# Kernel optimization log

Measured on AMD Instinct MI355X. Metric: run time of the kernel, lower is better.

## Reference

```python
import jax, jax.numpy as jnp
import numpy as np

B, T, D = 8, 1024, 1024
F, NB, FPB, ES, NE = 64, 4, 16, 4, 16
DFE, DRH, DEH = 128, 256, 512
RIN = D + DFE  # router input dim (hidden + feature embedding)
TEMP = 1.0
BUNDLE_TOPK = 2
EXPERT_TOPK = 2
LN_EPS = 1e-5


def setup_inputs() -> dict:
    key = jax.random.key(0)
    ks = jax.random.split(key, 24)
    s = 0.02
    n = lambda k, shp, sc=s: jax.random.normal(k, shp, dtype=jnp.float32) * sc
    return {
        "hidden": jax.random.normal(ks[0], (B, T, D), dtype=jnp.float32),
        "feat": jax.random.uniform(ks[1], (B, T, F), dtype=jnp.float32),
        "ln_g": jnp.ones((D,), jnp.float32),
        "ln_b": jnp.zeros((D,), jnp.float32),
        "stage_W": n(ks[2], (F, DFE)),
        "stage_b": jnp.zeros((DFE,), jnp.float32),
        "bproj_W": n(ks[3], (NB, FPB, DFE)),
        "bproj_b": jnp.zeros((NB, DFE), jnp.float32),
        "br_W1": n(ks[4], (RIN, DRH)),
        "br_b1": jnp.zeros((DRH,), jnp.float32),
        "br_W2": n(ks[5], (DRH, NB)),
        "br_b2": jnp.zeros((NB,), jnp.float32),
        "ir_W1": n(ks[6], (NB, RIN, DRH)),
        "ir_b1": jnp.zeros((NB, DRH), jnp.float32),
        "ir_W2": n(ks[7], (NB, DRH, ES)),
        "ir_b2": jnp.zeros((NB, ES), jnp.float32),
        "ex_W1": n(ks[8], (NE, D, DEH)),
        "ex_b1": jnp.zeros((NE, DEH), jnp.float32),
        "ex_W2": n(ks[9], (NE, DEH, D)),
        "ex_b2": jnp.zeros((NE, D), jnp.float32),
        "alpha": jnp.float32(1.0),
    }


def _topk_softmax(logits, temp, k):
    # scale by temperature, keep top-k logits, softmax (renormalized over kept)
    s = logits / temp
    if k is not None and k < s.shape[-1]:
        thr = jax.lax.top_k(s, k)[0][..., -1:]
        s = jnp.where(s >= thr, s, -jnp.inf)
    return jax.nn.softmax(s, axis=-1)


def _gelu(x):
    return jax.nn.gelu(x, approximate=False)  # torch nn.GELU default = exact erf


def reference(hidden, feat, ln_g, ln_b, stage_W, stage_b, bproj_W, bproj_b,
              br_W1, br_b1, br_W2, br_b2, ir_W1, ir_b1, ir_W2, ir_b2,
              ex_W1, ex_b1, ex_W2, ex_b2, alpha):
    # pre-LN
    mu = hidden.mean(-1, keepdims=True)
    var = ((hidden - mu) ** 2).mean(-1, keepdims=True)
    h_norm = (hidden - mu) * jax.lax.rsqrt(var + LN_EPS) * ln_g + ln_b  # [B,T,D]

    # stage feature embedding (stage_feat_idx = all 64 features here)
    sfe = feat @ stage_W + stage_b  # [B,T,DFE]
    bundle_in = jnp.concatenate([h_norm, sfe], axis=-1)  # [B,T,RIN]
    bundle_logits = _gelu(bundle_in @ br_W1 + br_b1) @ br_W2 + br_b2  # [B,T,NB]
    bundle_weights = _topk_softmax(bundle_logits, TEMP, BUNDLE_TOPK)

    # intra-bundle routers (vectorized over the 4 bundles)
    # bundle_feat_idx_g = [g*16 .. g*16+15] -> contiguous reshape is exact gather
    bfeat = feat.reshape(B, T, NB, FPB)
    bemb = jnp.einsum('btgf,gfe->btge', bfeat, bproj_W) + bproj_b  # [B,T,NB,DFE]
    iin = jnp.concatenate(
        [jnp.broadcast_to(h_norm[:, :, None, :], (B, T, NB, D)), bemb], axis=-1)
    ih = _gelu(jnp.einsum('btgi,gih->btgh', iin, ir_W1) + ir_b1)
    intra_logits = jnp.einsum('btgh,ghe->btge', ih, ir_W2) + ir_b2  # [B,T,NB,ES]
    intra_weights = _topk_softmax(intra_logits, TEMP, EXPERT_TOPK)

    gate_weights = (bundle_weights[..., None] * intra_weights).reshape(B, T, NE)
    gate_logits = (bundle_logits[..., None] + intra_logits).reshape(B, T, NE)

    # all experts run densely on h_norm, combined by gate weights
    eh = _gelu(jnp.einsum('btd,edh->bteh', h_norm, ex_W1) + ex_b1)  # [B,T,NE,DEH]
    eo = jnp.einsum('bteh,ehd->bted', eh, ex_W2) + ex_b2            # [B,T,NE,D]
    stage_delta = jnp.einsum('bte,bted->btd', gate_weights, eo)

    next_hidden = hidden + alpha * stage_delta  # alpha_scale = 1.0, eval dropout
    return (next_hidden, gate_weights, gate_logits, bundle_weights,
            bundle_logits, stage_delta)
```

## Files before the change

### kernel.cpp

```cpp
#include <hip/hip_runtime.h>


typedef unsigned short u16;
typedef u16 u16x8 __attribute__((ext_vector_type(8)));
typedef __bf16 bf16x8 __attribute__((ext_vector_type(8)));
typedef float f32x4 __attribute__((ext_vector_type(4)));

#define M_TOK 8192

__device__ __forceinline__ float bf2f(u16 u) {
  return __uint_as_float(((unsigned)u) << 16);
}
__device__ __forceinline__ u16 f2bf(float f) {
  unsigned u = __float_as_uint(f);
  unsigned r = (u + 0x7fffu + ((u >> 16) & 1u)) >> 16;
  return (u16)r;
}
__device__ __forceinline__ void split3(float x, u16& p0, u16& p1, u16& p2) {
  p0 = f2bf(x);
  float r = x - bf2f(p0);
  p1 = f2bf(r);
  float r2 = r - bf2f(p1);
  p2 = f2bf(r2);
}
__device__ __forceinline__ float gelu_exact(float x) {
  return 0.5f * x * (1.f + erff(x * 0.70710678118654752f));
}
__device__ __forceinline__ void gload16(const u16* g, u16* l) {
  __builtin_amdgcn_global_load_lds(
      (const __attribute__((address_space(1))) void*)g,
      (__attribute__((address_space(3))) void*)l, 16, 0, 0);
}

#define BAR()                               \
  do {                                      \
    asm volatile("" ::: "memory");          \
    __builtin_amdgcn_s_barrier();           \
    asm volatile("" ::: "memory");          \
  } while (0)
#define WAITV6() asm volatile("s_waitcnt vmcnt(6)" ::: "memory")
#define WAITV0() asm volatile("s_waitcnt vmcnt(0)" ::: "memory")

__global__ void probe_k(int* flag) {
  int lane = threadIdx.x & 63;
  int lq = lane & 15, quad = lane >> 4;
  u16x8 au, bu;
#pragma unroll
  for (int j = 0; j < 8; ++j) {
    int k = quad * 8 + j;
    float av = (k == 0) ? (float)lq : (k == 1 ? 1.f : 0.f);
    float bv = (k == 0) ? 1.f : (k == 1 ? 2.f * (float)lq : 0.f);
    au[j] = f2bf(av);
    bu[j] = f2bf(bv);
  }
  f32x4 acc = {};
  acc = __builtin_amdgcn_mfma_f32_16x16x32_bf16(
      __builtin_bit_cast(bf16x8, au), __builtin_bit_cast(bf16x8, bu), acc, 0, 0, 0);
  bool okg = true, oks = true;
#pragma unroll
  for (int rr = 0; rr < 4; ++rr) {
    float vg = (float)((quad * 4 + rr) + 2 * lq);
    float vs = (float)(lq + 2 * (quad * 4 + rr));
    okg = okg && (acc[rr] == vg);
    oks = oks && (acc[rr] == vs);
  }
  unsigned long long bg = __ballot(okg), bs = __ballot(oks);
  if (threadIdx.x == 0) *flag = (bg == ~0ull) ? 0 : ((bs == ~0ull) ? 1 : 0);
}

__global__ __launch_bounds__(256) void transpose_k(const float* __restrict__ src,
                                                   u16* __restrict__ dst,
                                                   int R, int C) {
  src += (size_t)blockIdx.z * R * C;
  dst += (size_t)blockIdx.z * R * C;
  __shared__ u16 tile[32][33];
  int r0 = blockIdx.x * 32, c0 = blockIdx.y * 32;
  int tx = threadIdx.x, ty = threadIdx.y;
#pragma unroll
  for (int k = 0; k < 4; ++k) {
    int r = r0 + ty + k * 8;
    if (r < R && c0 + tx < C) tile[ty + k * 8][tx] = f2bf(src[(size_t)r * C + c0 + tx]);
  }
  __syncthreads();
#pragma unroll
  for (int k = 0; k < 4; ++k) {
    int c = c0 + ty + k * 8;
    if (c < C && r0 + tx < R) dst[(size_t)c * R + r0 + tx] = tile[tx][ty + k * 8];
  }
}

__global__ __launch_bounds__(256) void transpose_k3(const float* __restrict__ src,
                                                    u16* __restrict__ dst,
                                                    int R, int C, size_t PS) {
  src += (size_t)blockIdx.z * R * C;
  dst += (size_t)blockIdx.z * R * C;
  __shared__ float tile[32][33];
  int r0 = blockIdx.x * 32, c0 = blockIdx.y * 32;
  int tx = threadIdx.x, ty = threadIdx.y;
#pragma unroll
  for (int k = 0; k < 4; ++k) {
    int r = r0 + ty + k * 8;
    if (r < R && c0 + tx < C) tile[ty + k * 8][tx] = src[(size_t)r * C + c0 + tx];
  }
  __syncthreads();
#pragma unroll
  for (int k = 0; k < 4; ++k) {
    int c = c0 + ty + k * 8;
    if (c < C && r0 + tx < R) {
      u16 p0, p1, p2;
      split3(tile[tx][ty + k * 8], p0, p1, p2);
      size_t idx = (size_t)c * R + r0 + tx;
      dst[idx] = p0;
      dst[PS + idx] = p1;
      dst[2 * PS + idx] = p2;
    }
  }
}

__global__ __launch_bounds__(256) void ln_k(const float* __restrict__ h,
                                            const float* __restrict__ gam,
                                            const float* __restrict__ bet,
                                            u16* __restrict__ out) {
  const size_t PS = (size_t)M_TOK * 1024;
  int wave = threadIdx.x >> 6, lane = threadIdx.x & 63;
  int t = blockIdx.x * 4 + wave;
  const float4* row4 = (const float4*)(h + (size_t)t * 1024);
  float x[16];
#pragma unroll
  for (int k = 0; k < 4; ++k) {
    float4 v = row4[lane * 4 + k];
    x[k * 4 + 0] = v.x; x[k * 4 + 1] = v.y; x[k * 4 + 2] = v.z; x[k * 4 + 3] = v.w;
  }
  float s = 0.f, ss = 0.f;
#pragma unroll
  for (int i = 0; i < 16; ++i) { s += x[i]; ss += x[i] * x[i]; }
#pragma unroll
  for (int m = 1; m < 64; m <<= 1) { s += __shfl_xor(s, m); ss += __shfl_xor(ss, m); }
  float mu = s * (1.f / 1024.f);
  float var = ss * (1.f / 1024.f) - mu * mu;
  float inv = rsqrtf(var + 1e-5f);
  const float4* g4 = (const float4*)gam;
  const float4* b4 = (const float4*)bet;
  u16x8 o0[3], o1[3];
#pragma unroll
  for (int k = 0; k < 4; ++k) {
    float4 g = g4[lane * 4 + k];
    float4 b = b4[lane * 4 + k];
    float vals[4] = {(x[k * 4 + 0] - mu) * inv * g.x + b.x,
                     (x[k * 4 + 1] - mu) * inv * g.y + b.y,
                     (x[k * 4 + 2] - mu) * inv * g.z + b.z,
                     (x[k * 4 + 3] - mu) * inv * g.w + b.w};
#pragma unroll
    for (int e = 0; e < 4; ++e) {
      u16 p0, p1, p2;
      split3(vals[e], p0, p1, p2);
      int sl = k * 4 + e;
      if (sl < 8) { o0[0][sl] = p0; o0[1][sl] = p1; o0[2][sl] = p2; }
      else { o1[0][sl - 8] = p0; o1[1][sl - 8] = p1; o1[2][sl - 8] = p2; }
    }
  }
  size_t base = (size_t)t * 1024 + lane * 16;
#pragma unroll
  for (int p = 0; p < 3; ++p) {
    *(u16x8*)(out + p * PS + base) = o0[p];
    *(u16x8*)(out + p * PS + base + 8) = o1[p];
  }
}

__global__ __launch_bounds__(128) void feat_k(const float* __restrict__ feat,
    const float* __restrict__ stW, const float* __restrict__ stb,
    const float* __restrict__ bpW, const float* __restrict__ bpb,
    u16* __restrict__ sfe3, u16* __restrict__ bemb3) {
  const size_t S_PS = (size_t)M_TOK * 128;
  const size_t E_PS = (size_t)4 * M_TOK * 128;
  int t = blockIdx.x;
  int n = threadIdx.x;
  __shared__ float fsh[64];
  if (n < 64) fsh[n] = feat[(size_t)t * 64 + n];
  __syncthreads();
  float s = stb[n];
  for (int k = 0; k < 64; ++k) s += fsh[k] * stW[k * 128 + n];
  {
    u16 p0, p1, p2;
    split3(s, p0, p1, p2);
    size_t idx = (size_t)t * 128 + n;
    sfe3[idx] = p0; sfe3[S_PS + idx] = p1; sfe3[2 * S_PS + idx] = p2;
  }
#pragma unroll
  for (int g = 0; g < 4; ++g) {
    float v = bpb[g * 128 + n];
#pragma unroll
    for (int j = 0; j < 16; ++j)
      v += fsh[g * 16 + j] * bpW[(g * 16 + j) * 128 + n];
    u16 p0, p1, p2;
    split3(v, p0, p1, p2);
    size_t idx = ((size_t)g * M_TOK + t) * 128 + n;
    bemb3[idx] = p0; bemb3[E_PS + idx] = p1; bemb3[2 * E_PS + idx] = p2;
  }
}

__global__ __launch_bounds__(256) void rgemm_k(
    const u16* __restrict__ hn3, const u16* __restrict__ sfe3,
    const u16* __restrict__ bemb3, const u16* __restrict__ Bt3,
    const float* __restrict__ bias0, const float* __restrict__ bias1,
    float* __restrict__ ih, const int* __restrict__ flagp) {
  __shared__ __align__(16) u16 shA[3][64 * 64];
  __shared__ __align__(16) u16 shB[3][64 * 64];
  const int tid = threadIdx.x;
  const int wave = tid >> 6, lane = tid & 63;
  const int gz = blockIdx.x >> 2;
  const int bn64 = (blockIdx.x & 3) * 64;
  const int bm64 = blockIdx.y * 64;
  const size_t A_PS = (size_t)M_TOK * 1024;
  const size_t S_PS = (size_t)M_TOK * 128;
  const size_t E_PS = (size_t)4 * M_TOK * 128;
  const size_t B_PS = (size_t)5 * 256 * 1152;
  const u16* AexB = (gz == 0) ? sfe3 : (bemb3 + (size_t)(gz - 1) * M_TOK * 128);
  const size_t Aex_PS = (gz == 0) ? S_PS : E_PS;
  const u16* BtP = Bt3 + (size_t)gz * 256 * 1152;

  f32x4 acc[2][2] = {};
  const int lq = lane & 15, quad = lane >> 4;
  const int wm = (wave >> 1) * 32, wn = (wave & 1) * 32;

  for (int kit = 0; kit < 18; ++kit) {
    int k0 = kit * 64;
#pragma unroll
    for (int half = 0; half < 2; ++half) {
      int ch = half * 256 + tid;
      int r = ch >> 3, ssl = ch & 7;
      int c = ssl ^ (r & 7);
      int gk = k0 + c * 8;
#pragma unroll
      for (int p = 0; p < 3; ++p) {
        const u16* gA = (gk < 1024)
            ? (hn3 + (size_t)p * A_PS + (size_t)(bm64 + r) * 1024 + gk)
            : (AexB + (size_t)p * Aex_PS + (size_t)(bm64 + r) * 128 + (gk - 1024));
        const u16* gB = BtP + (size_t)p * B_PS + (size_t)(bn64 + r) * 1152 + gk;
        gload16(gA, &shA[p][(half * 256 + wave * 64) * 8]);
        gload16(gB, &shB[p][(half * 256 + wave * 64) * 8]);
      }
    }
    __syncthreads();
#pragma unroll
    for (int ks = 0; ks < 2; ++ks) {
      bf16x8 af[3][2], bfr[3][2];
#pragma unroll
      for (int i = 0; i < 2; ++i) {
        int r = wm + i * 16 + lq;
        int cc = (ks * 4 + quad) ^ (r & 7);
        int rb = wn + i * 16 + lq;
        int cb = (ks * 4 + quad) ^ (rb & 7);
#pragma unroll
        for (int p = 0; p < 3; ++p) {
          af[p][i] = *(const bf16x8*)&shA[p][(r * 8 + cc) * 8];
          bfr[p][i] = *(const bf16x8*)&shB[p][(rb * 8 + cb) * 8];
        }
      }
#pragma unroll
      for (int i = 0; i < 2; ++i)
#pragma unroll
        for (int j = 0; j < 2; ++j) {
          acc[i][j] = __builtin_amdgcn_mfma_f32_16x16x32_bf16(af[0][i], bfr[0][j], acc[i][j], 0, 0, 0);
          acc[i][j] = __builtin_amdgcn_mfma_f32_16x16x32_bf16(af[0][i], bfr[1][j], acc[i][j], 0, 0, 0);
          acc[i][j] = __builtin_amdgcn_mfma_f32_16x16x32_bf16(af[1][i], bfr[0][j], acc[i][j], 0, 0, 0);
          acc[i][j] = __builtin_amdgcn_mfma_f32_16x16x32_bf16(af[0][i], bfr[2][j], acc[i][j], 0, 0, 0);
          acc[i][j] = __builtin_amdgcn_mfma_f32_16x16x32_bf16(af[1][i], bfr[1][j], acc[i][j], 0, 0, 0);
          acc[i][j] = __builtin_amdgcn_mfma_f32_16x16x32_bf16(af[2][i], bfr[0][j], acc[i][j], 0, 0, 0);
        }
    }
    __syncthreads();
  }

  const int fl = *flagp;
  const float* biasP = (gz == 0) ? bias0 : (bias1 + (gz - 1) * 256);
#pragma unroll
  for (int i = 0; i < 2; ++i) {
#pragma unroll
    for (int j = 0; j < 2; ++j) {
#pragma unroll
      for (int rr = 0; rr < 4; ++rr) {
        int m, col;
        if (fl == 0) {
          m = bm64 + wm + i * 16 + quad * 4 + rr;
          col = bn64 + wn + j * 16 + lq;
        } else {
          m = bm64 + wm + i * 16 + lq;
          col = bn64 + wn + j * 16 + quad * 4 + rr;
        }
        ih[((size_t)gz * M_TOK + m) * 256 + col] = gelu_exact(acc[i][j][rr] + biasP[col]);
      }
    }
  }
}

__global__ __launch_bounds__(512, 2) void ffn1_k(
    const u16* __restrict__ A0, const u16* __restrict__ Bt0,
    const float* __restrict__ b1all, const float* __restrict__ gwf,
    u16* __restrict__ out16, int e0, const int* __restrict__ flagp) {
  __shared__ __align__(16) u16 ldsA[2][2][128 * 64];
  __shared__ __align__(16) u16 ldsB[2][2][128 * 64];
  const int tid = threadIdx.x;
  const int wid = tid >> 6, lane = tid & 63;
  const int lq = lane & 15, quad = lane >> 4;
  const int swz = lq & 7;
  const int wmb = (wid >> 2) * 64;
  const int wnb = (wid & 3) * 32;
  const int ez = blockIdx.x >> 1;
  const int bn = (blockIdx.x & 1) * 256;
  const int bm = blockIdx.y * 256;
  const u16* BtP = Bt0 + (size_t)ez * 512 * 1024;

  f32x4 acc[8][4] = {};
  bf16x8 af[4][2], bfr[4][2];

  auto stageA = [&](int tt, int h) {
#pragma unroll
    for (int q = 0; q < 2; ++q) {
      int ch = q * 512 + tid;
      int r = ch >> 3, ssl = ch & 7;
      int c = ssl ^ (r & 7);
      gload16(A0 + (size_t)(bm + h * 128 + r) * 1024 + tt * 64 + c * 8,
              &ldsA[tt & 1][h][(q * 512 + (tid & ~63)) * 8]);
    }
  };
  auto stageB = [&](int tt, int h) {
#pragma unroll
    for (int q = 0; q < 2; ++q) {
      int ch = q * 512 + tid;
      int r = ch >> 3, ssl = ch & 7;
      int c = ssl ^ (r & 7);
      gload16(BtP + (size_t)(bn + h * 128 + r) * 1024 + tt * 64 + c * 8,
              &ldsB[tt & 1][h][(q * 512 + (tid & ~63)) * 8]);
    }
  };

  stageA(0, 0); stageB(0, 0); stageB(0, 1); stageA(0, 1);
  stageA(1, 0); stageB(1, 0); stageB(1, 1);
  WAITV6();
  BAR();

#pragma unroll 2
  for (int t = 0; t < 16; ++t) {
    const int buf = t & 1;
#pragma unroll
    for (int i = 0; i < 4; ++i) {
      int rh = wmb + i * 16 + lq;
#pragma unroll
      for (int ks = 0; ks < 2; ++ks)
        af[i][ks] = *(const bf16x8*)&ldsA[buf][0][(rh * 8 + ((ks * 4 + quad) ^ swz)) * 8];
    }
#pragma unroll
    for (int g = 0; g < 4; ++g) {
      int rh = wnb + (g & 1) * 16 + lq;
#pragma unroll
      for (int ks = 0; ks < 2; ++ks)
        bfr[g][ks] = *(const bf16x8*)&ldsB[buf][g >> 1][(rh * 8 + ((ks * 4 + quad) ^ swz)) * 8];
    }
    if (t + 1 < 16) stageA(t + 1, 1);
    BAR();
    __builtin_amdgcn_s_setprio(1);
#pragma unroll
    for (int i = 0; i < 4; ++i)
#pragma unroll
      for (int g = 0; g < 2; ++g) {
        acc[i][g] = __builtin_amdgcn_mfma_f32_16x16x32_bf16(af[i][0], bfr[g][0], acc[i][g], 0, 0, 0);
        acc[i][g] = __builtin_amdgcn_mfma_f32_16x16x32_bf16(af[i][1], bfr[g][1], acc[i][g], 0, 0, 0);
      }
    __builtin_amdgcn_s_setprio(0);
    BAR();
    if (t + 2 < 16) stageA(t + 2, 0);
    BAR();
    __builtin_amdgcn_s_setprio(1);
#pragma unroll
    for (int i = 0; i < 4; ++i)
#pragma unroll
      for (int g = 2; g < 4; ++g) {
        acc[i][g] = __builtin_amdgcn_mfma_f32_16x16x32_bf16(af[i][0], bfr[g][0], acc[i][g], 0, 0, 0);
        acc[i][g] = __builtin_amdgcn_mfma_f32_16x16x32_bf16(af[i][1], bfr[g][1], acc[i][g], 0, 0, 0);
      }
    __builtin_amdgcn_s_setprio(0);
    BAR();
#pragma unroll
    for (int i = 0; i < 4; ++i) {
      int rh = wmb + i * 16 + lq;
#pragma unroll
      for (int ks = 0; ks < 2; ++ks)
        af[i][ks] = *(const bf16x8*)&ldsA[buf][1][(rh * 8 + ((ks * 4 + quad) ^ swz)) * 8];
    }
    if (t + 2 < 16) stageB(t + 2, 0);
    BAR();
    __builtin_amdgcn_s_setprio(1);
#pragma unroll
    for (int i = 0; i < 4; ++i)
#pragma unroll
      for (int g = 0; g < 2; ++g) {
        acc[4 + i][g] = __builtin_amdgcn_mfma_f32_16x16x32_bf16(af[i][0], bfr[g][0], acc[4 + i][g], 0, 0, 0);
        acc[4 + i][g] = __builtin_amdgcn_mfma_f32_16x16x32_bf16(af[i][1], bfr[g][1], acc[4 + i][g], 0, 0, 0);
      }
    __builtin_amdgcn_s_setprio(0);
    BAR();
    if (t + 2 < 16) stageB(t + 2, 1);
    BAR();
    __builtin_amdgcn_s_setprio(1);
#pragma unroll
    for (int i = 0; i < 4; ++i)
#pragma unroll
      for (int g = 2; g < 4; ++g) {
        acc[4 + i][g] = __builtin_amdgcn_mfma_f32_16x16x32_bf16(af[i][0], bfr[g][0], acc[4 + i][g], 0, 0, 0);
        acc[4 + i][g] = __builtin_amdgcn_mfma_f32_16x16x32_bf16(af[i][1], bfr[g][1], acc[4 + i][g], 0, 0, 0);
      }
    __builtin_amdgcn_s_setprio(0);
    if (t == 14) { WAITV0(); } else { WAITV6(); }
    BAR();
  }

  const int fl = *flagp;
  const float* biasP = b1all + (e0 + ez) * 512;
#pragma unroll
  for (int f = 0; f < 8; ++f) {
    int mbase = bm + wmb + (f & 3) * 16 + (f >> 2) * 128;
#pragma unroll
    for (int g = 0; g < 4; ++g) {
      int cbase = bn + wnb + (g & 1) * 16 + (g >> 1) * 128;
#pragma unroll
      for (int rr = 0; rr < 4; ++rr) {
        int m, col;
        if (fl == 0) {
          m = mbase + quad * 4 + rr;
          col = cbase + lq;
        } else {
          m = mbase + lq;
          col = cbase + quad * 4 + rr;
        }
        float w = gwf[(size_t)m * 16 + e0 + ez];
        out16[((size_t)ez * M_TOK + m) * 512 + col] =
            f2bf(w * gelu_exact(acc[f][g][rr] + biasP[col]));
      }
    }
  }
}

__global__ __launch_bounds__(512, 2) void ffn2_k(
    const u16* __restrict__ A0, const u16* __restrict__ Bt0,
    float* __restrict__ outD, float* __restrict__ outP,
    int first, const int* __restrict__ flagp) {
  __shared__ __align__(16) u16 ldsA[2][2][128 * 64];
  __shared__ __align__(16) u16 ldsB[2][2][128 * 64];
  const int tid = threadIdx.x;
  const int wid = tid >> 6, lane = tid & 63;
  const int lq = lane & 15, quad = lane >> 4;
  const int swz = lq & 7;
  const int wmb = (wid >> 2) * 64;
  const int wnb = (wid & 3) * 32;
  const int kz = blockIdx.x & 1;
  const int bn = (blockIdx.x >> 1) * 256;
  const int bm = blockIdx.y * 256;

  f32x4 acc[8][4] = {};
  bf16x8 af[4][2], bfr[4][2];

  auto stageA = [&](int tt, int h) {
#pragma unroll
    for (int q = 0; q < 2; ++q) {
      int ch = q * 512 + tid;
      int r = ch >> 3, ssl = ch & 7;
      int c = ssl ^ (r & 7);
      int el = kz * 4 + (tt >> 3), kk = (tt & 7) * 64 + c * 8;
      gload16(A0 + ((size_t)el * M_TOK + bm + h * 128 + r) * 512 + kk,
              &ldsA[tt & 1][h][(q * 512 + (tid & ~63)) * 8]);
    }
  };
  auto stageB = [&](int tt, int h) {
#pragma unroll
    for (int q = 0; q < 2; ++q) {
      int ch = q * 512 + tid;
      int r = ch >> 3, ssl = ch & 7;
      int c = ssl ^ (r & 7);
      int el = kz * 4 + (tt >> 3), kk = (tt & 7) * 64 + c * 8;
      gload16(Bt0 + ((size_t)el * 1024 + bn + h * 128 + r) * 512 + kk,
              &ldsB[tt & 1][h][(q * 512 + (tid & ~63)) * 8]);
    }
  };

  stageA(0, 0); stageB(0, 0); stageB(0, 1); stageA(0, 1);
  stageA(1, 0); stageB(1, 0); stageB(1, 1);
  WAITV6();
  BAR();

#pragma unroll 2
  for (int t = 0; t < 32; ++t) {
    const int buf = t & 1;
#pragma unroll
    for (int i = 0; i < 4; ++i) {
      int rh = wmb + i * 16 + lq;
#pragma unroll
      for (int ks = 0; ks < 2; ++ks)
        af[i][ks] = *(const bf16x8*)&ldsA[buf][0][(rh * 8 + ((ks * 4 + quad) ^ swz)) * 8];
    }
#pragma unroll
    for (int g = 0; g < 4; ++g) {
      int rh = wnb + (g & 1) * 16 + lq;
#pragma unroll
      for (int ks = 0; ks < 2; ++ks)
        bfr[g][ks] = *(const bf16x8*)&ldsB[buf][g >> 1][(rh * 8 + ((ks * 4 + quad) ^ swz)) * 8];
    }
    if (t + 1 < 32) stageA(t + 1, 1);
    BAR();
    __builtin_amdgcn_s_setprio(1);
#pragma unroll
    for (int i = 0; i < 4; ++i)
#pragma unroll
      for (int g = 0; g < 2; ++g) {
        acc[i][g] = __builtin_amdgcn_mfma_f32_16x16x32_bf16(af[i][0], bfr[g][0], acc[i][g], 0, 0, 0);
        acc[i][g] = __builtin_amdgcn_mfma_f32_16x16x32_bf16(af[i][1], bfr[g][1], acc[i][g], 0, 0, 0);
      }
    __builtin_amdgcn_s_setprio(0);
    BAR();
    if (t + 2 < 32) stageA(t + 2, 0);
    BAR();
    __builtin_amdgcn_s_setprio(1);
#pragma unroll
    for (int i = 0; i < 4; ++i)
#pragma unroll
      for (int g = 2; g < 4; ++g) {
        acc[i][g] = __builtin_amdgcn_mfma_f32_16x16x32_bf16(af[i][0], bfr[g][0], acc[i][g], 0, 0, 0);
        acc[i][g] = __builtin_amdgcn_mfma_f32_16x16x32_bf16(af[i][1], bfr[g][1], acc[i][g], 0, 0, 0);
      }
    __builtin_amdgcn_s_setprio(0);
    BAR();
#pragma unroll
    for (int i = 0; i < 4; ++i) {
      int rh = wmb + i * 16 + lq;
#pragma unroll
      for (int ks = 0; ks < 2; ++ks)
        af[i][ks] = *(const bf16x8*)&ldsA[buf][1][(rh * 8 + ((ks * 4 + quad) ^ swz)) * 8];
    }
    if (t + 2 < 32) stageB(t + 2, 0);
    BAR();
    __builtin_amdgcn_s_setprio(1);
#pragma unroll
    for (int i = 0; i < 4; ++i)
#pragma unroll
      for (int g = 0; g < 2; ++g) {
        acc[4 + i][g] = __builtin_amdgcn_mfma_f32_16x16x32_bf16(af[i][0], bfr[g][0], acc[4 + i][g], 0, 0, 0);
        acc[4 + i][g] = __builtin_amdgcn_mfma_f32_16x16x32_bf16(af[i][1], bfr[g][1], acc[4 + i][g], 0, 0, 0);
      }
    __builtin_amdgcn_s_setprio(0);
    BAR();
    if (t + 2 < 32) stageB(t + 2, 1);
    BAR();
    __builtin_amdgcn_s_setprio(1);
#pragma unroll
    for (int i = 0; i < 4; ++i)
#pragma unroll
      for (int g = 2; g < 4; ++g) {
        acc[4 + i][g] = __builtin_amdgcn_mfma_f32_16x16x32_bf16(af[i][0], bfr[g][0], acc[4 + i][g], 0, 0, 0);
        acc[4 + i][g] = __builtin_amdgcn_mfma_f32_16x16x32_bf16(af[i][1], bfr[g][1], acc[4 + i][g], 0, 0, 0);
      }
    __builtin_amdgcn_s_setprio(0);
    if (t == 30) { WAITV0(); } else { WAITV6(); }
    BAR();
  }

  const int fl = *flagp;
  float* outp = kz ? outP : outD;
#pragma unroll
  for (int f = 0; f < 8; ++f) {
    int mbase = bm + wmb + (f & 3) * 16 + (f >> 2) * 128;
#pragma unroll
    for (int g = 0; g < 4; ++g) {
      int cbase = bn + wnb + (g & 1) * 16 + (g >> 1) * 128;
#pragma unroll
      for (int rr = 0; rr < 4; ++rr) {
        int m, col;
        if (fl == 0) {
          m = mbase + quad * 4 + rr;
          col = cbase + lq;
        } else {
          m = mbase + lq;
          col = cbase + quad * 4 + rr;
        }
        size_t idx = (size_t)m * 1024 + col;
        float v = acc[f][g][rr];
        outp[idx] = first ? v : (outp[idx] + v);
      }
    }
  }
}

__device__ __forceinline__ void topk2_softmax4(const float* s, float* w) {
  float m1 = fmaxf(fmaxf(s[0], s[1]), fmaxf(s[2], s[3]));
  float m2 = -1e30f;
  bool seen = false;
#pragma unroll
  for (int i = 0; i < 4; ++i) {
    if (s[i] == m1 && !seen) seen = true;
    else m2 = fmaxf(m2, s[i]);
  }
  float e[4];
  float sum = 0.f;
#pragma unroll
  for (int i = 0; i < 4; ++i) {
    e[i] = (s[i] >= m2) ? expf(s[i] - m1) : 0.f;
    sum += e[i];
  }
  float invs = 1.f / sum;
#pragma unroll
  for (int i = 0; i < 4; ++i) w[i] = e[i] * invs;
}

__global__ __launch_bounds__(256) void gating_k(
    const float* __restrict__ ih_all, const float* __restrict__ brW2,
    const float* __restrict__ brb2, const float* __restrict__ irW2,
    const float* __restrict__ irb2, float* __restrict__ gwf,
    float* __restrict__ o_gw, float* __restrict__ o_gl,
    float* __restrict__ o_bw, float* __restrict__ o_bl) {
  int wave = threadIdx.x >> 6, lane = threadIdx.x & 63;
  int t = blockIdx.x * 4 + wave;
  const float4* bw4 = (const float4*)brW2;
  const float4* iw4 = (const float4*)irW2;
  float v[20];
#pragma unroll
  for (int i = 0; i < 20; ++i) v[i] = 0.f;
  const float* bh = ih_all + (size_t)t * 256;
#pragma unroll
  for (int jj = 0; jj < 4; ++jj) {
    int k = jj * 64 + lane;
    float h = bh[k];
    float4 wv = bw4[k];
    v[0] += h * wv.x; v[1] += h * wv.y; v[2] += h * wv.z; v[3] += h * wv.w;
  }
#pragma unroll
  for (int g = 0; g < 4; ++g) {
    const float* ihg = ih_all + ((size_t)(1 + g) * M_TOK + t) * 256;
#pragma unroll
    for (int jj = 0; jj < 4; ++jj) {
      int k = jj * 64 + lane;
      float h = ihg[k];
      float4 wv = iw4[g * 256 + k];
      v[4 + g * 4 + 0] += h * wv.x; v[4 + g * 4 + 1] += h * wv.y;
      v[4 + g * 4 + 2] += h * wv.z; v[4 + g * 4 + 3] += h * wv.w;
    }
  }
#pragma unroll
  for (int i = 0; i < 20; ++i)
#pragma unroll
    for (int m = 1; m < 64; m <<= 1) v[i] += __shfl_xor(v[i], m);
  if (lane == 0) {
    float blog[4], ilog[4][4];
#pragma unroll
    for (int c = 0; c < 4; ++c) blog[c] = v[c] + brb2[c];
#pragma unroll
    for (int g = 0; g < 4; ++g)
#pragma unroll
      for (int e = 0; e < 4; ++e) ilog[g][e] = v[4 + g * 4 + e] + irb2[g * 4 + e];
    float bw[4];
    topk2_softmax4(blog, bw);
#pragma unroll
    for (int g = 0; g < 4; ++g) {
      float iw[4];
      topk2_softmax4(ilog[g], iw);
#pragma unroll
      for (int e = 0; e < 4; ++e) {
        int idx = g * 4 + e;
        float wv = bw[g] * iw[e];
        gwf[(size_t)t * 16 + idx] = wv;
        o_gw[(size_t)t * 16 + idx] = wv;
        o_gl[(size_t)t * 16 + idx] = blog[g] + ilog[g][e];
      }
      o_bw[(size_t)t * 4 + g] = bw[g];
      o_bl[(size_t)t * 4 + g] = blog[g];
    }
  }
}

__global__ __launch_bounds__(256) void combine_k(
    const float* __restrict__ gwf, const float* __restrict__ b2,
    const float* __restrict__ hidden, const float* __restrict__ alpha_p,
    const float* __restrict__ part,
    float* __restrict__ o_next, float* __restrict__ o_delta) {
  int row = blockIdx.x;
  float a = alpha_p[0];
  float wb[16];
#pragma unroll
  for (int e = 0; e < 16; ++e) wb[e] = gwf[(size_t)row * 16 + e];
#pragma unroll
  for (int k = 0; k < 4; ++k) {
    int c = threadIdx.x + k * 256;
    float s = 0.f;
#pragma unroll
    for (int e = 0; e < 16; ++e) s += wb[e] * b2[e * 1024 + c];
    size_t idx = (size_t)row * 1024 + c;
    float d = o_delta[idx] + part[idx] + s;
    o_delta[idx] = d;
    o_next[idx] = hidden[idx] + a * d;
  }
}

extern "C" void kernel_launch(void* const* d_in, const int* in_sizes, int n_in,
                              void* d_out, int out_size, void* d_ws, size_t ws_size,
                              hipStream_t stream) {
  (void)in_sizes; (void)n_in; (void)out_size; (void)ws_size;
  const float* hidden  = (const float*)d_in[0];
  const float* feat    = (const float*)d_in[1];
  const float* ln_g    = (const float*)d_in[2];
  const float* ln_b    = (const float*)d_in[3];
  const float* stage_W = (const float*)d_in[4];
  const float* stage_b = (const float*)d_in[5];
  const float* bproj_W = (const float*)d_in[6];
  const float* bproj_b = (const float*)d_in[7];
  const float* br_W1   = (const float*)d_in[8];
  const float* br_b1   = (const float*)d_in[9];
  const float* br_W2   = (const float*)d_in[10];
  const float* br_b2   = (const float*)d_in[11];
  const float* ir_W1   = (const float*)d_in[12];
  const float* ir_b1   = (const float*)d_in[13];
  const float* ir_W2   = (const float*)d_in[14];
  const float* ir_b2   = (const float*)d_in[15];
  const float* ex_W1   = (const float*)d_in[16];
  const float* ex_b1   = (const float*)d_in[17];
  const float* ex_W2   = (const float*)d_in[18];
  const float* ex_b2   = (const float*)d_in[19];
  const float* alpha   = (const float*)d_in[20];

  char* w = (char*)d_ws;
  size_t off = 0;
  auto alloc = [&](size_t bytes) {
    void* p = w + off;
    off += (bytes + 255) & ~(size_t)255;
    return p;
  };
  int* flagp   = (int*)alloc(256);
  u16* wt3     = (u16*)alloc(3ull * 5 * 256 * 1152 * 2);
  u16* hn3     = (u16*)alloc(3ull * M_TOK * 1024 * 2);
  float* gwf   = (float*)alloc((size_t)M_TOK * 16 * 4);
  char* region = (char*)alloc(88090000);
  u16* sfe3   = (u16*)region;
  u16* bemb3  = (u16*)(region + 6291456);
  float* ih   = (float*)(region + 6291456 + 25165824);
  u16* w1t_g  = (u16*)region;
  u16* w2t_g  = (u16*)(region + 8388608);
  u16* Gbuf   = (u16*)(region + 16777216);
  float* o_part1 = (float*)(((char*)hn3) + (size_t)M_TOK * 1024 * 2);

  float* out = (float*)d_out;
  float* o_next  = out;
  float* o_gw    = out + 8388608;
  float* o_gl    = o_gw + 131072;
  float* o_bw    = o_gl + 131072;
  float* o_bl    = o_bw + 32768;
  float* o_delta = o_bl + 32768;

  probe_k<<<1, 64, 0, stream>>>(flagp);

  transpose_k3<<<dim3(36, 8, 1), dim3(32, 8), 0, stream>>>(
      br_W1, wt3, 1152, 256, (size_t)5 * 256 * 1152);
  transpose_k3<<<dim3(36, 8, 4), dim3(32, 8), 0, stream>>>(
      ir_W1, wt3 + 256 * 1152, 1152, 256, (size_t)5 * 256 * 1152);

  ln_k<<<2048, 256, 0, stream>>>(hidden, ln_g, ln_b, hn3);
  feat_k<<<8192, 128, 0, stream>>>(feat, stage_W, stage_b, bproj_W, bproj_b, sfe3, bemb3);

  rgemm_k<<<dim3(20, 128), 256, 0, stream>>>(hn3, sfe3, bemb3, wt3, br_b1, ir_b1, ih, flagp);
  gating_k<<<2048, 256, 0, stream>>>(ih, br_W2, br_b2, ir_W2, ir_b2, gwf,
                                     o_gw, o_gl, o_bw, o_bl);

  for (int grp = 0; grp < 2; ++grp) {
    transpose_k<<<dim3(32, 16, 8), dim3(32, 8), 0, stream>>>(
        ex_W1 + (size_t)grp * 8 * 1024 * 512, w1t_g, 1024, 512);
    transpose_k<<<dim3(16, 32, 8), dim3(32, 8), 0, stream>>>(
        ex_W2 + (size_t)grp * 8 * 512 * 1024, w2t_g, 512, 1024);
    ffn1_k<<<dim3(16, 32), 512, 0, stream>>>(hn3, w1t_g, ex_b1, gwf,
                                             Gbuf, grp * 8, flagp);
    ffn2_k<<<dim3(8, 32), 512, 0, stream>>>(Gbuf, w2t_g, o_delta, o_part1,
                                            grp == 0 ? 1 : 0, flagp);
  }

  combine_k<<<8192, 256, 0, stream>>>(gwf, ex_b2, hidden, alpha, o_part1,
                                      o_next, o_delta);
}
```

Before: 813.5 us.

## Pipeline router GEMM with double-buffered LDS and larger 128-row tiles

After: 851.4 us. +4.7%, slower.

```diff
diff --git a/kernel.cpp b/kernel.cpp
--- a/kernel.cpp
+++ b/kernel.cpp
@@ -38,6 +38,7 @@
     __builtin_amdgcn_s_barrier();           \
     asm volatile("" ::: "memory");          \
   } while (0)
+#define WAITV8() asm volatile("s_waitcnt vmcnt(8)" ::: "memory")
 #define WAITV6() asm volatile("s_waitcnt vmcnt(6)" ::: "memory")
 #define WAITV0() asm volatile("s_waitcnt vmcnt(0)" ::: "memory")
 
@@ -199,18 +200,19 @@
   }
 }
 
-__global__ __launch_bounds__(256) void rgemm_k(
+__global__ __launch_bounds__(512, 2) void rgemm_k(
     const u16* __restrict__ hn3, const u16* __restrict__ sfe3,
     const u16* __restrict__ bemb3, const u16* __restrict__ Bt3,
     const float* __restrict__ bias0, const float* __restrict__ bias1,
     float* __restrict__ ih, const int* __restrict__ flagp) {
-  __shared__ __align__(16) u16 shA[3][64 * 64];
-  __shared__ __align__(16) u16 shB[3][64 * 64];
+  __shared__ __align__(16) u16 ldsA[2][3][128 * 64];
+  __shared__ __align__(16) u16 ldsB[2][3][64 * 64];
   const int tid = threadIdx.x;
-  const int wave = tid >> 6, lane = tid & 63;
+  const int wid = tid >> 6, lane = tid & 63;
+  const int lq = lane & 15, quad = lane >> 4;
   const int gz = blockIdx.x >> 2;
-  const int bn64 = (blockIdx.x & 3) * 64;
-  const int bm64 = blockIdx.y * 64;
+  const int bn = (blockIdx.x & 3) * 64;
+  const int bm = blockIdx.y * 128;
   const size_t A_PS = (size_t)M_TOK * 1024;
   const size_t S_PS = (size_t)M_TOK * 128;
   const size_t E_PS = (size_t)4 * M_TOK * 128;
@@ -219,57 +221,132 @@
   const size_t Aex_PS = (gz == 0) ? S_PS : E_PS;
   const u16* BtP = Bt3 + (size_t)gz * 256 * 1152;
 
+  const int wm = (wid >> 1) * 32, wn = (wid & 1) * 32;
+
   f32x4 acc[2][2] = {};
-  const int lq = lane & 15, quad = lane >> 4;
-  const int wm = (wave >> 1) * 32, wn = (wave & 1) * 32;
-
-  for (int kit = 0; kit < 18; ++kit) {
-    int k0 = kit * 64;
-#pragma unroll
-    for (int half = 0; half < 2; ++half) {
-      int ch = half * 256 + tid;
+  bf16x8 af0[2][2], af1[2][2], af2[2][2];
+  bf16x8 bf0[2][2], bf1[2][2], bf2[2][2];
+
+  auto stageA = [&](int p, int tt) {
+#pragma unroll
+    for (int q = 0; q < 2; ++q) {
+      int ch = q * 512 + tid;
       int r = ch >> 3, ssl = ch & 7;
       int c = ssl ^ (r & 7);
-      int gk = k0 + c * 8;
-#pragma unroll
-      for (int p = 0; p < 3; ++p) {
-        const u16* gA = (gk < 1024)
-            ? (hn3 + (size_t)p * A_PS + (size_t)(bm64 + r) * 1024 + gk)
-            : (AexB + (size_t)p * Aex_PS + (size_t)(bm64 + r) * 128 + (gk - 1024));
-        const u16* gB = BtP + (size_t)p * B_PS + (size_t)(bn64 + r) * 1152 + gk;
-        gload16(gA, &shA[p][(half * 256 + wave * 64) * 8]);
-        gload16(gB, &shB[p][(half * 256 + wave * 64) * 8]);
-      }
-    }
-    __syncthreads();
-#pragma unroll
-    for (int ks = 0; ks < 2; ++ks) {
-      bf16x8 af[3][2], bfr[3][2];
-#pragma unroll
-      for (int i = 0; i < 2; ++i) {
-        int r = wm + i * 16 + lq;
+      int gk = tt * 64 + c * 8;
+      const u16* gA = (gk < 1024)
+          ? (hn3 + (size_t)p * A_PS + (size_t)(bm + r) * 1024 + gk)
+          : (AexB + (size_t)p * Aex_PS + (size_t)(bm + r) * 128 + (gk - 1024));
+      gload16(gA, &ldsA[tt & 1][p][(q * 512 + (tid & ~63)) * 8]);
+    }
+  };
+  auto stageB = [&](int p, int tt) {
+    int r = tid >> 3, ssl = tid & 7;
+    int c = ssl ^ (r & 7);
+    int gk = tt * 64 + c * 8;
+    gload16(BtP + (size_t)p * B_PS + (size_t)(bn + r) * 1152 + gk,
+            &ldsB[tt & 1][p][(tid & ~63) * 8]);
+  };
+
+  stageA(0, 0); stageA(1, 0); stageA(2, 0);
+  stageB(0, 0); stageB(1, 0); stageB(2, 0);
+  stageA(0, 1); stageA(1, 1);
+  stageB(0, 1); stageB(1, 1); stageA(2, 1);
+  WAITV8();
+  BAR();
+
+#pragma unroll 2
+  for (int t = 0; t < 18; ++t) {
+    const int buf = t & 1;
+#pragma unroll
+    for (int i = 0; i < 2; ++i) {
+      int r = wm + i * 16 + lq;
+#pragma unroll
+      for (int ks = 0; ks < 2; ++ks) {
         int cc = (ks * 4 + quad) ^ (r & 7);
-        int rb = wn + i * 16 + lq;
+        af0[i][ks] = *(const bf16x8*)&ldsA[buf][0][(r * 8 + cc) * 8];
+        af1[i][ks] = *(const bf16x8*)&ldsA[buf][1][(r * 8 + cc) * 8];
+      }
+    }
+#pragma unroll
+    for (int j = 0; j < 2; ++j) {
+      int rb = wn + j * 16 + lq;
+#pragma unroll
+      for (int ks = 0; ks < 2; ++ks) {
         int cb = (ks * 4 + quad) ^ (rb & 7);
-#pragma unroll
-        for (int p = 0; p < 3; ++p) {
-          af[p][i] = *(const bf16x8*)&shA[p][(r * 8 + cc) * 8];
-          bfr[p][i] = *(const bf16x8*)&shB[p][(rb * 8 + cb) * 8];
+        bf0[j][ks] = *(const bf16x8*)&ldsB[buf][0][(rb * 8 + cb) * 8];
+      }
+    }
+    if (t + 1 < 18) stageB(2, t + 1);
+    BAR();
+    __builtin_amdgcn_s_setprio(1);
+#pragma unroll
+    for (int i = 0; i < 2; ++i)
+#pragma unroll
+      for (int j = 0; j < 2; ++j)
+#pragma unroll
+        for (int ks = 0; ks < 2; ++ks) {
+          acc[i][j] = __builtin_amdgcn_mfma_f32_16x16x32_bf16(af0[i][ks], bf0[j][ks], acc[i][j], 0, 0, 0);
+          acc[i][j] = __builtin_amdgcn_mfma_f32_16x16x32_bf16(af1[i][ks], bf0[j][ks], acc[i][j], 0, 0, 0);
         }
-      }
-#pragma unroll
-      for (int i = 0; i < 2; ++i)
-#pragma unroll
-        for (int j = 0; j < 2; ++j) {
-          acc[i][j] = __builtin_amdgcn_mfma_f32_16x16x32_bf16(af[0][i], bfr[0][j], acc[i][j], 0, 0, 0);
-          acc[i][j] = __builtin_amdgcn_mfma_f32_16x16x32_bf16(af[0][i], bfr[1][j], acc[i][j], 0, 0, 0);
-          acc[i][j] = __builtin_amdgcn_mfma_f32_16x16x32_bf16(af[1][i], bfr[0][j], acc[i][j], 0, 0, 0);
-          acc[i][j] = __builtin_amdgcn_mfma_f32_16x16x32_bf16(af[0][i], bfr[2][j], acc[i][j], 0, 0, 0);
-          acc[i][j] = __builtin_amdgcn_mfma_f32_16x16x32_bf16(af[1][i], bfr[1][j], acc[i][j], 0, 0, 0);
-          acc[i][j] = __builtin_amdgcn_mfma_f32_16x16x32_bf16(af[2][i], bfr[0][j], acc[i][j], 0, 0, 0);
+    __builtin_amdgcn_s_setprio(0);
+    BAR();
+#pragma unroll
+    for (int j = 0; j < 2; ++j) {
+      int rb = wn + j * 16 + lq;
+#pragma unroll
+      for (int ks = 0; ks < 2; ++ks) {
+        int cb = (ks * 4 + quad) ^ (rb & 7);
+        bf1[j][ks] = *(const bf16x8*)&ldsB[buf][1][(rb * 8 + cb) * 8];
+      }
+    }
+#pragma unroll
+    for (int i = 0; i < 2; ++i) {
+      int r = wm + i * 16 + lq;
+#pragma unroll
+      for (int ks = 0; ks < 2; ++ks) {
+        int cc = (ks * 4 + quad) ^ (r & 7);
+        af2[i][ks] = *(const bf16x8*)&ldsA[buf][2][(r * 8 + cc) * 8];
+      }
+    }
+    if (t + 2 < 18) { stageA(0, t + 2); stageA(1, t + 2); }
+    BAR();
+    __builtin_amdgcn_s_setprio(1);
+#pragma unroll
+    for (int i = 0; i < 2; ++i)
+#pragma unroll
+      for (int j = 0; j < 2; ++j)
+#pragma unroll
+        for (int ks = 0; ks < 2; ++ks) {
+          acc[i][j] = __builtin_amdgcn_mfma_f32_16x16x32_bf16(af0[i][ks], bf1[j][ks], acc[i][j], 0, 0, 0);
+          acc[i][j] = __builtin_amdgcn_mfma_f32_16x16x32_bf16(af1[i][ks], bf1[j][ks], acc[i][j], 0, 0, 0);
         }
-    }
-    __syncthreads();
+    __builtin_amdgcn_s_setprio(0);
+    BAR();
+#pragma unroll
+    for (int j = 0; j < 2; ++j) {
+      int rb = wn + j * 16 + lq;
+#pragma unroll
+      for (int ks = 0; ks < 2; ++ks) {
+        int cb = (ks * 4 + quad) ^ (rb & 7);
+        bf2[j][ks] = *(const bf16x8*)&ldsB[buf][2][(rb * 8 + cb) * 8];
+      }
+    }
+    if (t + 2 < 18) { stageB(0, t + 2); stageB(1, t + 2); stageA(2, t + 2); }
+    BAR();
+    __builtin_amdgcn_s_setprio(1);
+#pragma unroll
+    for (int i = 0; i < 2; ++i)
+#pragma unroll
+      for (int j = 0; j < 2; ++j)
+#pragma unroll
+        for (int ks = 0; ks < 2; ++ks) {
+          acc[i][j] = __builtin_amdgcn_mfma_f32_16x16x32_bf16(af2[i][ks], bf0[j][ks], acc[i][j], 0, 0, 0);
+          acc[i][j] = __builtin_amdgcn_mfma_f32_16x16x32_bf16(af0[i][ks], bf2[j][ks], acc[i][j], 0, 0, 0);
+        }
+    __builtin_amdgcn_s_setprio(0);
+    if (t == 16) { WAITV0(); } else if (t < 16) { WAITV8(); }
+    BAR();
   }
 
   const int fl = *flagp;
@@ -282,11 +359,11 @@
       for (int rr = 0; rr < 4; ++rr) {
         int m, col;
         if (fl == 0) {
-          m = bm64 + wm + i * 16 + quad * 4 + rr;
-          col = bn64 + wn + j * 16 + lq;
+          m = bm + wm + i * 16 + quad * 4 + rr;
+          col = bn + wn + j * 16 + lq;
         } else {
-          m = bm64 + wm + i * 16 + lq;
-          col = bn64 + wn + j * 16 + quad * 4 + rr;
+          m = bm + wm + i * 16 + lq;
+          col = bn + wn + j * 16 + quad * 4 + rr;
         }
         ih[((size_t)gz * M_TOK + m) * 256 + col] = gelu_exact(acc[i][j][rr] + biasP[col]);
       }
@@ -762,7 +839,7 @@
   ln_k<<<2048, 256, 0, stream>>>(hidden, ln_g, ln_b, hn3);
   feat_k<<<8192, 128, 0, stream>>>(feat, stage_W, stage_b, bproj_W, bproj_b, sfe3, bemb3);
 
-  rgemm_k<<<dim3(20, 128), 256, 0, stream>>>(hn3, sfe3, bemb3, wt3, br_b1, ir_b1, ih, flagp);
+  rgemm_k<<<dim3(20, 64), 512, 0, stream>>>(hn3, sfe3, bemb3, wt3, br_b1, ir_b1, ih, flagp);
   gating_k<<<2048, 256, 0, stream>>>(ih, br_W2, br_b2, ir_W2, ir_b2, gwf,
                                      o_gw, o_gl, o_bw, o_bl);
 
```

## Switch router GEMM from 3-way bf16 split to 2-way scaled fp16 split

Applied to the files above, without the earlier changes.

Result: faster. 787.3 us (-3.2%).

```diff
diff --git a/kernel.cpp b/kernel.cpp
--- a/kernel.cpp
+++ b/kernel.cpp
@@ -4,6 +4,8 @@
 typedef unsigned short u16;
 typedef u16 u16x8 __attribute__((ext_vector_type(8)));
 typedef __bf16 bf16x8 __attribute__((ext_vector_type(8)));
+typedef _Float16 f16;
+typedef f16 f16x8 __attribute__((ext_vector_type(8)));
 typedef float f32x4 __attribute__((ext_vector_type(4)));
 
 #define M_TOK 8192
@@ -16,12 +18,17 @@
   unsigned r = (u + 0x7fffu + ((u >> 16) & 1u)) >> 16;
   return (u16)r;
 }
-__device__ __forceinline__ void split3(float x, u16& p0, u16& p1, u16& p2) {
-  p0 = f2bf(x);
-  float r = x - bf2f(p0);
-  p1 = f2bf(r);
-  float r2 = r - bf2f(p1);
-  p2 = f2bf(r2);
+__device__ __forceinline__ u16 f2h(float f) {
+  f16 h = (f16)f;
+  return __builtin_bit_cast(u16, h);
+}
+__device__ __forceinline__ float h2f(u16 u) {
+  return (float)__builtin_bit_cast(f16, u);
+}
+__device__ __forceinline__ void split2h(float x, u16& p0, u16& p1) {
+  p0 = f2h(x);
+  float r = x - h2f(p0);
+  p1 = f2h(r * 2048.f);
 }
 __device__ __forceinline__ float gelu_exact(float x) {
   return 0.5f * x * (1.f + erff(x * 0.70710678118654752f));
@@ -89,9 +96,9 @@
   }
 }
 
-__global__ __launch_bounds__(256) void transpose_k3(const float* __restrict__ src,
-                                                    u16* __restrict__ dst,
-                                                    int R, int C, size_t PS) {
+__global__ __launch_bounds__(256) void transpose_k2h(const float* __restrict__ src,
+                                                     u16* __restrict__ dst,
+                                                     int R, int C, size_t PS) {
   src += (size_t)blockIdx.z * R * C;
   dst += (size_t)blockIdx.z * R * C;
   __shared__ float tile[32][33];
@@ -107,12 +114,11 @@
   for (int k = 0; k < 4; ++k) {
     int c = c0 + ty + k * 8;
     if (c < C && r0 + tx < R) {
-      u16 p0, p1, p2;
-      split3(tile[tx][ty + k * 8], p0, p1, p2);
+      u16 p0, p1;
+      split2h(tile[tx][ty + k * 8], p0, p1);
       size_t idx = (size_t)c * R + r0 + tx;
       dst[idx] = p0;
       dst[PS + idx] = p1;
-      dst[2 * PS + idx] = p2;
     }
   }
 }
@@ -152,11 +158,12 @@
                      (x[k * 4 + 3] - mu) * inv * g.w + b.w};
 #pragma unroll
     for (int e = 0; e < 4; ++e) {
-      u16 p0, p1, p2;
-      split3(vals[e], p0, p1, p2);
+      u16 pb = f2bf(vals[e]);
+      u16 q0, q1;
+      split2h(vals[e], q0, q1);
       int sl = k * 4 + e;
-      if (sl < 8) { o0[0][sl] = p0; o0[1][sl] = p1; o0[2][sl] = p2; }
-      else { o1[0][sl - 8] = p0; o1[1][sl - 8] = p1; o1[2][sl - 8] = p2; }
+      if (sl < 8) { o0[0][sl] = pb; o0[1][sl] = q0; o0[2][sl] = q1; }
+      else { o1[0][sl - 8] = pb; o1[1][sl - 8] = q0; o1[2][sl - 8] = q1; }
     }
   }
   size_t base = (size_t)t * 1024 + lane * 16;
@@ -181,10 +188,10 @@
   float s = stb[n];
   for (int k = 0; k < 64; ++k) s += fsh[k] * stW[k * 128 + n];
   {
-    u16 p0, p1, p2;
-    split3(s, p0, p1, p2);
+    u16 p0, p1;
+    split2h(s, p0, p1);
     size_t idx = (size_t)t * 128 + n;
-    sfe3[idx] = p0; sfe3[S_PS + idx] = p1; sfe3[2 * S_PS + idx] = p2;
+    sfe3[idx] = p0; sfe3[S_PS + idx] = p1;
   }
 #pragma unroll
   for (int g = 0; g < 4; ++g) {
@@ -192,20 +199,20 @@
 #pragma unroll
     for (int j = 0; j < 16; ++j)
       v += fsh[g * 16 + j] * bpW[(g * 16 + j) * 128 + n];
-    u16 p0, p1, p2;
-    split3(v, p0, p1, p2);
+    u16 p0, p1;
+    split2h(v, p0, p1);
     size_t idx = ((size_t)g * M_TOK + t) * 128 + n;
-    bemb3[idx] = p0; bemb3[E_PS + idx] = p1; bemb3[2 * E_PS + idx] = p2;
+    bemb3[idx] = p0; bemb3[E_PS + idx] = p1;
   }
 }
 
 __global__ __launch_bounds__(256) void rgemm_k(
-    const u16* __restrict__ hn3, const u16* __restrict__ sfe3,
-    const u16* __restrict__ bemb3, const u16* __restrict__ Bt3,
+    const u16* __restrict__ hnF, const u16* __restrict__ sfe2,
+    const u16* __restrict__ bemb2, const u16* __restrict__ Bt2,
     const float* __restrict__ bias0, const float* __restrict__ bias1,
     float* __restrict__ ih, const int* __restrict__ flagp) {
-  __shared__ __align__(16) u16 shA[3][64 * 64];
-  __shared__ __align__(16) u16 shB[3][64 * 64];
+  __shared__ __align__(16) u16 shA[2][64 * 64];
+  __shared__ __align__(16) u16 shB[2][64 * 64];
   const int tid = threadIdx.x;
   const int wave = tid >> 6, lane = tid & 63;
   const int gz = blockIdx.x >> 2;
@@ -215,11 +222,11 @@
   const size_t S_PS = (size_t)M_TOK * 128;
   const size_t E_PS = (size_t)4 * M_TOK * 128;
   const size_t B_PS = (size_t)5 * 256 * 1152;
-  const u16* AexB = (gz == 0) ? sfe3 : (bemb3 + (size_t)(gz - 1) * M_TOK * 128);
+  const u16* AexB = (gz == 0) ? sfe2 : (bemb2 + (size_t)(gz - 1) * M_TOK * 128);
   const size_t Aex_PS = (gz == 0) ? S_PS : E_PS;
-  const u16* BtP = Bt3 + (size_t)gz * 256 * 1152;
-
-  f32x4 acc[2][2] = {};
+  const u16* BtP = Bt2 + (size_t)gz * 256 * 1152;
+
+  f32x4 acc[2][2][2] = {};
   const int lq = lane & 15, quad = lane >> 4;
   const int wm = (wave >> 1) * 32, wn = (wave & 1) * 32;
 
@@ -232,9 +239,9 @@
       int c = ssl ^ (r & 7);
       int gk = k0 + c * 8;
 #pragma unroll
-      for (int p = 0; p < 3; ++p) {
+      for (int p = 0; p < 2; ++p) {
         const u16* gA = (gk < 1024)
-            ? (hn3 + (size_t)p * A_PS + (size_t)(bm64 + r) * 1024 + gk)
+            ? (hnF + (size_t)p * A_PS + (size_t)(bm64 + r) * 1024 + gk)
             : (AexB + (size_t)p * Aex_PS + (size_t)(bm64 + r) * 128 + (gk - 1024));
         const u16* gB = BtP + (size_t)p * B_PS + (size_t)(bn64 + r) * 1152 + gk;
         gload16(gA, &shA[p][(half * 256 + wave * 64) * 8]);
@@ -244,7 +251,7 @@
     __syncthreads();
 #pragma unroll
     for (int ks = 0; ks < 2; ++ks) {
-      bf16x8 af[3][2], bfr[3][2];
+      f16x8 af[2][2], bfr[2][2];
 #pragma unroll
       for (int i = 0; i < 2; ++i) {
         int r = wm + i * 16 + lq;
@@ -252,21 +259,18 @@
         int rb = wn + i * 16 + lq;
         int cb = (ks * 4 + quad) ^ (rb & 7);
 #pragma unroll
-        for (int p = 0; p < 3; ++p) {
-          af[p][i] = *(const bf16x8*)&shA[p][(r * 8 + cc) * 8];
-          bfr[p][i] = *(const bf16x8*)&shB[p][(rb * 8 + cb) * 8];
+        for (int p = 0; p < 2; ++p) {
+          af[p][i] = *(const f16x8*)&shA[p][(r * 8 + cc) * 8];
+          bfr[p][i] = *(const f16x8*)&shB[p][(rb * 8 + cb) * 8];
         }
       }
 #pragma unroll
       for (int i = 0; i < 2; ++i)
 #pragma unroll
         for (int j = 0; j < 2; ++j) {
-          acc[i][j] = __builtin_amdgcn_mfma_f32_16x16x32_bf16(af[0][i], bfr[0][j], acc[i][j], 0, 0, 0);
-          acc[i][j] = __builtin_amdgcn_mfma_f32_16x16x32_bf16(af[0][i], bfr[1][j], acc[i][j], 0, 0, 0);
-          acc[i][j] = __builtin_amdgcn_mfma_f32_16x16x32_bf16(af[1][i], bfr[0][j], acc[i][j], 0, 0, 0);
-          acc[i][j] = __builtin_amdgcn_mfma_f32_16x16x32_bf16(af[0][i], bfr[2][j], acc[i][j], 0, 0, 0);
-          acc[i][j] = __builtin_amdgcn_mfma_f32_16x16x32_bf16(af[1][i], bfr[1][j], acc[i][j], 0, 0, 0);
-          acc[i][j] = __builtin_amdgcn_mfma_f32_16x16x32_bf16(af[2][i], bfr[0][j], acc[i][j], 0, 0, 0);
+          acc[i][j][0] = __builtin_amdgcn_mfma_f32_16x16x32_f16(af[0][i], bfr[0][j], acc[i][j][0], 0, 0, 0);
+          acc[i][j][1] = __builtin_amdgcn_mfma_f32_16x16x32_f16(af[0][i], bfr[1][j], acc[i][j][1], 0, 0, 0);
+          acc[i][j][1] = __builtin_amdgcn_mfma_f32_16x16x32_f16(af[1][i], bfr[0][j], acc[i][j][1], 0, 0, 0);
         }
     }
     __syncthreads();
@@ -288,7 +292,8 @@
           m = bm64 + wm + i * 16 + lq;
           col = bn64 + wn + j * 16 + quad * 4 + rr;
         }
-        ih[((size_t)gz * M_TOK + m) * 256 + col] = gelu_exact(acc[i][j][rr] + biasP[col]);
+        float v = acc[i][j][0][rr] + acc[i][j][1][rr] * (1.f / 2048.f);
+        ih[((size_t)gz * M_TOK + m) * 256 + col] = gelu_exact(v + biasP[col]);
       }
     }
   }
@@ -754,15 +759,16 @@
 
   probe_k<<<1, 64, 0, stream>>>(flagp);
 
-  transpose_k3<<<dim3(36, 8, 1), dim3(32, 8), 0, stream>>>(
+  transpose_k2h<<<dim3(36, 8, 1), dim3(32, 8), 0, stream>>>(
       br_W1, wt3, 1152, 256, (size_t)5 * 256 * 1152);
-  transpose_k3<<<dim3(36, 8, 4), dim3(32, 8), 0, stream>>>(
+  transpose_k2h<<<dim3(36, 8, 4), dim3(32, 8), 0, stream>>>(
       ir_W1, wt3 + 256 * 1152, 1152, 256, (size_t)5 * 256 * 1152);
 
   ln_k<<<2048, 256, 0, stream>>>(hidden, ln_g, ln_b, hn3);
   feat_k<<<8192, 128, 0, stream>>>(feat, stage_W, stage_b, bproj_W, bproj_b, sfe3, bemb3);
 
-  rgemm_k<<<dim3(20, 128), 256, 0, stream>>>(hn3, sfe3, bemb3, wt3, br_b1, ir_b1, ih, flagp);
+  rgemm_k<<<dim3(20, 128), 256, 0, stream>>>(hn3 + (size_t)M_TOK * 1024, sfe3, bemb3,
+                                             wt3, br_b1, ir_b1, ih, flagp);
   gating_k<<<2048, 256, 0, stream>>>(ih, br_W2, br_b2, ir_W2, ir_b2, gwf,
                                      o_gw, o_gl, o_bw, o_bl);
 
```
